# Performance work log

Hardware: AMD Instinct MI355X
Metric: run time of the kernel (lower is better)

Reference implementation:

```python
import jax, jax.numpy as jnp
import numpy as np

B, L, D_MODEL, HEADS, EXP, DEPTH = 2, 2048, 1024, 16, 2, 12
D_EXP = D_MODEL * EXP
D_HEAD = D_EXP // HEADS


def _layernorm(x, g, b, eps=1e-5):
    mu = jnp.mean(x, axis=-1, keepdims=True)
    var = jnp.mean(jnp.square(x - mu), axis=-1, keepdims=True)
    return (x - mu) * jax.lax.rsqrt(var + eps) * g + b


def setup_inputs() -> dict:
    key = jax.random.key(0)
    ks = jax.random.split(key, 4)
    x = jax.random.normal(ks[0], (B, L, D_MODEL), dtype=jnp.float32)
    w_in = jax.random.normal(ks[1], (D_MODEL, 4 * D_EXP), dtype=jnp.float32) * 0.02
    w_out = jax.random.normal(ks[2], (D_EXP, D_MODEL), dtype=jnp.float32) * (0.02 / np.sqrt(2 * DEPTH))
    return {
        "x": x,
        "ln1_g": jnp.ones((D_MODEL,), jnp.float32),
        "ln1_b": jnp.zeros((D_MODEL,), jnp.float32),
        "ln2_g": jnp.ones((D_MODEL,), jnp.float32),
        "ln2_b": jnp.zeros((D_MODEL,), jnp.float32),
        "w_in": w_in,
        "w_out": w_out,
        "smear_factor": jnp.linspace(-6.0, 6.0, HEADS, dtype=jnp.float32),
        "log_scale": jnp.zeros((HEADS,), jnp.float32),
    }


def reference(x, ln1_g, ln1_b, ln2_g, ln2_b, w_in, w_out, smear_factor, log_scale):
    b, l, d = x.shape
    h = smear_factor.shape[0]
    d_exp = w_in.shape[1] // 4
    dh = d_exp // h

    qkvp = _layernorm(x, ln1_g, ln1_b) @ w_in  # [b, l, 4*d_exp]
    q, k, v, p = jnp.split(qkvp, 4, axis=-1)
    # 'b i (h d) -> b h i d'
    to_heads = lambda t: t.reshape(b, l, h, dh).transpose(0, 2, 1, 3)
    q, k, v = to_heads(q), to_heads(k), to_heads(v)

    # smeared keys: k_i <- (1-s)*k_i + s*k_{i-1}  (zero at i=0)
    smear = jax.nn.sigmoid(smear_factor)[None, :, None, None]
    k_prev = jnp.pad(k, ((0, 0), (0, 0), (1, 0), (0, 0)))[:, :, :-1, :]
    k = (1.0 - smear) * k + smear * k_prev

    # ALiBi-style additive mask: slope[h]*j on causal part, -1e10 above diag
    half = h // 2
    slopes = jnp.concatenate([2.0 ** jnp.linspace(0.0, -8.0, half), jnp.zeros((h - half,), jnp.float32)])
    j = jnp.arange(l)
    causal = jnp.where(j[None, :] > j[:, None], jnp.float32(-1e10), jnp.float32(0.0))  # [l, l]
    mask = slopes[:, None, None] * j[None, None, :].astype(jnp.float32) + causal[None, :, :]  # [h, l, l]

    # SDPA with q/s, k/s and default scale 1/sqrt(dh): logits = q k^T / (s^2 sqrt(dh))
    inv = 1.0 / (jnp.exp(2.0 * log_scale)[None, :, None, None] * jnp.sqrt(jnp.float32(dh)))
    logits = jnp.einsum('bhid,bhjd->bhij', q, k) * inv + mask[None]
    attn = jax.nn.softmax(logits, axis=-1)
    o = jnp.einsum('bhij,bhjd->bhid', attn, v)
    o = o.transpose(0, 2, 1, 3).reshape(b, l, h * dh)  # 'b h i d -> b i (h d)'

    out = (jax.nn.silu(p) * o) @ w_out
    return _layernorm(out, ln2_g, ln2_b)
```

## Files before the change

### kernel.cpp

```cpp
#include <hip/hip_runtime.h>

typedef unsigned short u16;
typedef __attribute__((ext_vector_type(8))) short bf16x8;
typedef __attribute__((ext_vector_type(8))) unsigned short u16x8;
typedef __attribute__((ext_vector_type(4))) float f32x4;

#define L_SEQ 2048
#define NTOK 4096
#define DMODEL 1024
#define DEXP 2048
#define NH 16
#define DH 128

__device__ __forceinline__ u16 f2bf(float f) {
    unsigned u = __float_as_uint(f);
    unsigned r = (u + 0x7FFFu + ((u >> 16) & 1u)) >> 16;
    return (u16)r;
}
__device__ __forceinline__ float bf2f(u16 h) {
    return __uint_as_float(((unsigned)h) << 16);
}

template <int CTRL>
__device__ __forceinline__ float dpp_f(float x) {
    return __int_as_float(__builtin_amdgcn_update_dpp(0, __float_as_int(x), CTRL, 0xF, 0xF, true));
}
__device__ __forceinline__ float red16_max(float x) {
    x = fmaxf(x, dpp_f<0xB1>(x));
    x = fmaxf(x, dpp_f<0x4E>(x));
    x = fmaxf(x, dpp_f<0x124>(x));
    x = fmaxf(x, dpp_f<0x128>(x));
    return x;
}

__device__ __forceinline__ void gl_lds16(const u16* g, u16* l) {
    __builtin_amdgcn_global_load_lds((const __attribute__((address_space(1))) void*)g,
                                     (__attribute__((address_space(3))) void*)l, 16, 0, 0);
}

__global__ void conv_transpose(const float* __restrict__ in, u16* __restrict__ out, int R, int C) {
    __shared__ unsigned tile[32][33];
    int c0 = blockIdx.x * 32, r0 = blockIdx.y * 32;
    int tx = threadIdx.x, ty = threadIdx.y;
    for (int j = 0; j < 32; j += 8)
        tile[ty + j][tx] = (unsigned)f2bf(in[(size_t)(r0 + ty + j) * C + c0 + tx]);
    __syncthreads();
    for (int j = 0; j < 32; j += 8)
        out[(size_t)(c0 + ty + j) * R + r0 + tx] = (u16)tile[tx][ty + j];
}

__global__ __launch_bounds__(256) void ln_fwd(const float* __restrict__ x, const float* __restrict__ g,
                                              const float* __restrict__ bta, void* __restrict__ outp,
                                              int out_bf16) {
    int row = blockIdx.x;
    int t = threadIdx.x;
    const float* xr = x + (size_t)row * DMODEL;
    float4 xv = *(const float4*)&xr[t * 4];
    float s = xv.x + xv.y + xv.z + xv.w;
    float s2 = xv.x * xv.x + xv.y * xv.y + xv.z * xv.z + xv.w * xv.w;
    for (int off = 32; off >= 1; off >>= 1) {
        s += __shfl_xor(s, off);
        s2 += __shfl_xor(s2, off);
    }
    __shared__ float red[10];
    int w = t >> 6;
    if ((t & 63) == 0) { red[w] = s; red[4 + w] = s2; }
    __syncthreads();
    if (t == 0) {
        red[8] = red[0] + red[1] + red[2] + red[3];
        red[9] = red[4] + red[5] + red[6] + red[7];
    }
    __syncthreads();
    float mu = red[8] * (1.0f / DMODEL);
    float var = red[9] * (1.0f / DMODEL) - mu * mu;
    float rstd = rsqrtf(var + 1e-5f);
    float vals[4] = {xv.x, xv.y, xv.z, xv.w};
    for (int e = 0; e < 4; e++) {
        int c = t * 4 + e;
        float y = (vals[e] - mu) * rstd * g[c] + bta[c];
        if (out_bf16) ((u16*)outp)[(size_t)row * DMODEL + c] = f2bf(y);
        else          ((float*)outp)[(size_t)row * DMODEL + c] = y;
    }
}

__device__ __forceinline__ void store_out(u16* C, size_t idx, float v) { C[idx] = f2bf(v); }
__device__ __forceinline__ void store_out(float* C, size_t idx, float v) { C[idx] = v; }

template <typename OutT>
__global__ __launch_bounds__(256) void gemm_bt(const u16* __restrict__ A, const u16* __restrict__ BT,
                                               OutT* __restrict__ C, int M, int N, int K) {
    __shared__ u16 a_s[4096];
    __shared__ u16 b_s[4096];
    int tid = threadIdx.x;
    int m0 = blockIdx.y * 128, n0 = blockIdx.x * 128;
    int w = tid >> 6, lane = tid & 63, quad = lane >> 4, ln = lane & 15;
    int wr = (w >> 1) * 64, wc = (w & 1) * 64;
    f32x4 zero4 = {0.f, 0.f, 0.f, 0.f};
    f32x4 acc[4][4];
    for (int r = 0; r < 4; r++)
        for (int c = 0; c < 4; c++) acc[r][c] = zero4;

    int lrow = lane >> 2, lseg = (lane & 3) * 8;
    const u16* Ag0 = A + (size_t)(m0 + 32 * w + lrow) * K + lseg;
    const u16* Ag1 = Ag0 + (size_t)16 * K;
    const u16* Bg0 = BT + (size_t)(n0 + 32 * w + lrow) * K + lseg;
    const u16* Bg1 = Bg0 + (size_t)16 * K;
    u16* al0 = &a_s[(2 * w) * 512];
    u16* al1 = &a_s[(2 * w + 1) * 512];
    u16* bl0 = &b_s[(2 * w) * 512];
    u16* bl1 = &b_s[(2 * w + 1) * 512];

    for (int k0 = 0; k0 < K; k0 += 32) {
        __syncthreads();
        gl_lds16(Ag0 + k0, al0);
        gl_lds16(Ag1 + k0, al1);
        gl_lds16(Bg0 + k0, bl0);
        gl_lds16(Bg1 + k0, bl1);
        __syncthreads();
        bf16x8 af[4], bfr[4];
        for (int r = 0; r < 4; r++) af[r]  = *(const bf16x8*)&a_s[(wr + r * 16 + ln) * 32 + quad * 8];
        for (int c = 0; c < 4; c++) bfr[c] = *(const bf16x8*)&b_s[(wc + c * 16 + ln) * 32 + quad * 8];
        for (int r = 0; r < 4; r++)
            for (int c = 0; c < 4; c++)
                acc[r][c] = __builtin_amdgcn_mfma_f32_16x16x32_bf16(af[r], bfr[c], acc[r][c], 0, 0, 0);
    }
    for (int r = 0; r < 4; r++)
        for (int c = 0; c < 4; c++)
            for (int e = 0; e < 4; e++) {
                int row = m0 + wr + r * 16 + quad * 4 + e;
                int col = n0 + wc + c * 16 + ln;
                store_out(C, (size_t)row * N + col, acc[r][c][e]);
            }
}

__global__ __launch_bounds__(256) void smear_kernel(const u16* __restrict__ qkvp,
                                                    const float* __restrict__ smear_f,
                                                    u16* __restrict__ k_sm) {
    int gid = blockIdx.x * 256 + threadIdx.x;
    int base = gid * 8;
    int bl = base >> 11;
    int c = base & 2047;
    int h = c >> 7;
    int d = c & 127;
    int l = bl & (L_SEQ - 1);
    int bb = bl >> 11;
    float s = 1.0f / (1.0f + __expf(-smear_f[h]));
    u16x8 cur = *(const u16x8*)&qkvp[(size_t)bl * 8192 + 2048 + c];
    u16x8 prv = {0, 0, 0, 0, 0, 0, 0, 0};
    if (l > 0) prv = *(const u16x8*)&qkvp[(size_t)(bl - 1) * 8192 + 2048 + c];
    u16x8 outv;
    for (int u = 0; u < 8; u++) {
        float kc = bf2f(cur[u]);
        float kp = bf2f(prv[u]);
        outv[u] = f2bf((1.0f - s) * kc + s * kp);
    }
    *(u16x8*)&k_sm[(((size_t)(bb * 16 + h)) * L_SEQ + l) * DH + d] = outv;
}

__global__ void vT_kernel(const u16* __restrict__ qkvp, u16* __restrict__ v_t) {
    __shared__ unsigned tile[32][33];
    int l0 = blockIdx.x * 32, d0 = blockIdx.y * 32;
    int bh = blockIdx.z;
    int bb = bh >> 4, h = bh & 15;
    int tx = threadIdx.x, ty = threadIdx.y;
    size_t tokb = (size_t)bb * L_SEQ;
    for (int j = 0; j < 32; j += 8)
        tile[ty + j][tx] = (unsigned)qkvp[(tokb + l0 + ty + j) * 8192 + 4096 + h * DH + d0 + tx];
    __syncthreads();
    for (int j = 0; j < 32; j += 8)
        v_t[((size_t)bh * DH + d0 + ty + j) * L_SEQ + l0 + tx] = (u16)tile[tx][ty + j];
}

__global__ __launch_bounds__(256) void attn_kernel(const u16* __restrict__ qkvp,
                                                   const u16* __restrict__ k_sm,
                                                   const u16* __restrict__ v_t,
                                                   u16* __restrict__ ag2,
                                                   const float* __restrict__ log_scale) {
    __shared__ u16 k_s[8192];
    __shared__ u16 vt_s[8192];
    __shared__ u16 p_s[4608];
    int tid = threadIdx.x;
    int bh = blockIdx.y;
    int bb = bh >> 4, h = bh & 15;
    int w = tid >> 6, lane = tid & 63, quad = lane >> 4, ln = lane & 15;
    size_t tokb = (size_t)bb * L_SEQ;

    const float LOG2E = 1.44269504f;
    float inv = 1.0f / (__expf(2.0f * log_scale[h]) * sqrtf((float)DH));
    float scl = inv * LOG2E;
    float slope2 = ((h < 8) ? exp2f(-8.0f * (float)h / 7.0f) : 0.0f) * LOG2E;

    int lrow = lane >> 2, lseg8 = (lane & 3) * 8;
    f32x4 zero4 = {0.f, 0.f, 0.f, 0.f};
    u16* pw = &p_s[w * 1152];
    const short ONE_BF = (short)0x3F80;
    bf16x8 ones = {ONE_BF, ONE_BF, ONE_BF, ONE_BF, ONE_BF, ONE_BF, ONE_BF, ONE_BF};

    for (int sidx = 0; sidx < 2; sidx++) {
        int ib = sidx == 0 ? (31 - (int)blockIdx.x) : (int)blockIdx.x;
        int i0 = ib * 64;
        int si = i0 + w * 16;

        bf16x8 qf[4];
        for (int kt = 0; kt < 4; kt++)
            qf[kt] = *(const bf16x8*)&qkvp[(tokb + si + ln) * 8192 + h * DH + kt * 32 + quad * 8];

        float m_i[4];
        for (int r = 0; r < 4; r++) m_i[r] = -1e30f;
        f32x4 o_acc[8], l_acc;
        for (int dt = 0; dt < 8; dt++) o_acc[dt] = zero4;
        l_acc = zero4;

        const u16* kg[4];
        for (int g = 0; g < 4; g++)
            kg[g] = k_sm + ((size_t)bh * L_SEQ + g * 16 + lrow) * DH + w * 32 + lseg8;
        const u16* vg[4];
        u16* vl[4];
        for (int q = 0; q < 4; q++) {
            int c = w * 4 + q;
            int jt = c >> 3, dg = c & 7;
            vg[q] = v_t + ((size_t)bh * DH + dg * 16 + lrow) * L_SEQ + jt * 32 + lseg8;
            vl[q] = &vt_s[jt * 4096 + dg * 512];
        }

        for (int j0 = 0; j0 <= i0; j0 += 64) {
            __syncthreads();
            for (int g = 0; g < 4; g++) {
                gl_lds16(kg[g], &k_s[w * 2048 + g * 512]);
                kg[g] += 64 * DH;
            }
            for (int q = 0; q < 4; q++) {
                gl_lds16(vg[q], vl[q]);
                vg[q] += 64;
            }
            __syncthreads();
            if (j0 > si + 15) continue;

            f32x4 sc[4];
            for (int ct = 0; ct < 4; ct++) sc[ct] = zero4;
            for (int kt = 0; kt < 4; kt++)
                for (int ct = 0; ct < 4; ct++) {
                    bf16x8 bfr = *(const bf16x8*)&k_s[kt * 2048 + (ct * 16 + ln) * 32 + quad * 8];
                    sc[ct] = __builtin_amdgcn_mfma_f32_16x16x32_bf16(qf[kt], bfr, sc[ct], 0, 0, 0);
                }

            bool full = (j0 + 63 <= si);
            float s2[4][4];
            float aj0 = slope2 * (float)(j0 + ln);
            for (int ct = 0; ct < 4; ct++) {
                float ajv = aj0 + slope2 * (float)(16 * ct);
                int j = j0 + ct * 16 + ln;
                for (int r = 0; r < 4; r++) {
                    float v = fmaf(sc[ct][r], scl, ajv);
                    if (!full) {
                        int i = si + quad * 4 + r;
                        if (j > i) v = -3.0e38f;
                    }
                    s2[ct][r] = v;
                }
            }
            float alpha[4];
            bool any_resc = false;
            for (int r = 0; r < 4; r++) {
                float mr = fmaxf(fmaxf(s2[0][r], s2[1][r]), fmaxf(s2[2][r], s2[3][r]));
                mr = red16_max(mr);
                float mnew = fmaxf(m_i[r], mr);
                alpha[r] = exp2f(m_i[r] - mnew);
                any_resc |= (alpha[r] != 1.0f);
                m_i[r] = mnew;
                for (int ct = 0; ct < 4; ct++) {
                    float p = exp2f(s2[ct][r] - mnew);
                    u16 pb = (u16)(__float_as_uint(p) >> 16);
                    pw[(quad * 4 + r) * 72 + ct * 16 + ln] = pb;
                }
            }
            if (__any(any_resc)) {
                for (int dt = 0; dt < 8; dt++) {
                    f32x4 o = o_acc[dt];
                    for (int r = 0; r < 4; r++) o[r] *= alpha[r];
                    o_acc[dt] = o;
                }
                for (int r = 0; r < 4; r++) l_acc[r] *= alpha[r];
            }
            asm volatile("s_waitcnt lgkmcnt(0)" ::: "memory");
            for (int ks = 0; ks < 2; ks++) {
                bf16x8 pa = *(const bf16x8*)&pw[ln * 72 + ks * 32 + quad * 8];
                l_acc = __builtin_amdgcn_mfma_f32_16x16x32_bf16(pa, ones, l_acc, 0, 0, 0);
                for (int dt = 0; dt < 8; dt++) {
                    bf16x8 vf = *(const bf16x8*)&vt_s[ks * 4096 + (dt * 16 + ln) * 32 + quad * 8];
                    o_acc[dt] = __builtin_amdgcn_mfma_f32_16x16x32_bf16(pa, vf, o_acc[dt], 0, 0, 0);
                }
            }
        }

        float rinv[4];
        for (int r = 0; r < 4; r++) rinv[r] = __builtin_amdgcn_rcpf(l_acc[r]);
        for (int dt = 0; dt < 8; dt++)
            for (int r = 0; r < 4; r++) {
                int i = si + quad * 4 + r;
                int dcol = dt * 16 + ln;
                float o = o_acc[dt][r] * rinv[r];
                float pv = bf2f(qkvp[(tokb + i) * 8192 + 6144 + h * DH + dcol]);
                float gate = pv * __builtin_amdgcn_rcpf(1.0f + exp2f(-pv * LOG2E));
                ag2[(tokb + i) * 2048 + h * DH + dcol] = f2bf(gate * o);
            }
    }
}

extern "C" void kernel_launch(void* const* d_in, const int* in_sizes, int n_in,
                              void* d_out, int out_size, void* d_ws, size_t ws_size,
                              hipStream_t stream) {
    const float* x       = (const float*)d_in[0];
    const float* ln1_g   = (const float*)d_in[1];
    const float* ln1_b   = (const float*)d_in[2];
    const float* ln2_g   = (const float*)d_in[3];
    const float* ln2_b   = (const float*)d_in[4];
    const float* w_in    = (const float*)d_in[5];
    const float* w_out   = (const float*)d_in[6];
    const float* smear_f = (const float*)d_in[7];
    const float* logsc   = (const float*)d_in[8];
    float* out = (float*)d_out;
    char* ws = (char*)d_ws;

    u16* w_inT   = (u16*)(ws + 0);
    u16* w_outT  = (u16*)(ws + (size_t)16777216);
    u16* lnA     = (u16*)(ws + (size_t)20971520);
    u16* qkvp    = (u16*)(ws + (size_t)29360128);
    u16* k_sm    = (u16*)(ws + (size_t)96468992);
    u16* ag2     = (u16*)(ws + (size_t)113246208);
    float* out_pre = (float*)(ws + (size_t)96468992);
    u16* v_t     = (u16*)(ws + 0);

    dim3 b32x8(32, 8);
    conv_transpose<<<dim3(8192 / 32, 1024 / 32), b32x8, 0, stream>>>(w_in, w_inT, 1024, 8192);
    conv_transpose<<<dim3(1024 / 32, 2048 / 32), b32x8, 0, stream>>>(w_out, w_outT, 2048, 1024);
    ln_fwd<<<NTOK, 256, 0, stream>>>(x, ln1_g, ln1_b, (void*)lnA, 1);
    gemm_bt<u16><<<dim3(8192 / 128, 4096 / 128), 256, 0, stream>>>(lnA, w_inT, qkvp, NTOK, 8192, 1024);
    smear_kernel<<<4096, 256, 0, stream>>>(qkvp, smear_f, k_sm);
    vT_kernel<<<dim3(L_SEQ / 32, DH / 32, 32), b32x8, 0, stream>>>(qkvp, v_t);
    attn_kernel<<<dim3(16, 32), 256, 0, stream>>>(qkvp, k_sm, v_t, ag2, logsc);
    gemm_bt<float><<<dim3(1024 / 128, 4096 / 128), 256, 0, stream>>>(ag2, w_outT, out_pre, NTOK, 1024, 2048);
    ln_fwd<<<NTOK, 256, 0, stream>>>(out_pre, ln2_g, ln2_b, (void*)out, 0);
}
```

Baseline: 387.4 us.

## Double-buffer K/V tiles in LDS with XOR swizzle and MFMA priority hints

The attention kernel now keeps two LDS buffers for the K and V^T tiles. It prefetches the next 64-key tile while computing on the current one, which removes one of the two barriers per iteration. It also XOR-swizzles the 8-element column segments in LDS, by changing the global source addresses and the read offsets, to cut bank conflicts on the fragment reads. s_setprio is raised around the MFMA loops. The cost is double the K/V LDS footprint, which may lower occupancy, and the early skip of fully masked wave tiles is gone.

```diff
diff --git a/kernel.cpp b/kernel.cpp
--- a/kernel.cpp
+++ b/kernel.cpp
@@ -176,8 +176,8 @@
                                                    const u16* __restrict__ v_t,
                                                    u16* __restrict__ ag2,
                                                    const float* __restrict__ log_scale) {
-    __shared__ u16 k_s[8192];
-    __shared__ u16 vt_s[8192];
+    __shared__ u16 k_s[16384];
+    __shared__ u16 vt_s[16384];
     __shared__ u16 p_s[4608];
     int tid = threadIdx.x;
     int bh = blockIdx.y;
@@ -190,7 +190,9 @@
     float scl = inv * LOG2E;
     float slope2 = ((h < 8) ? exp2f(-8.0f * (float)h / 7.0f) : 0.0f) * LOG2E;
 
-    int lrow = lane >> 2, lseg8 = (lane & 3) * 8;
+    int lrow = lane >> 2, lcol = lane & 3;
+    int lsw8 = (lcol ^ ((lrow >> 1) & 3)) * 8;
+    int qsw = (quad ^ ((ln >> 1) & 3)) * 8;
     f32x4 zero4 = {0.f, 0.f, 0.f, 0.f};
     u16* pw = &p_s[w * 1152];
     const short ONE_BF = (short)0x3F80;
@@ -213,36 +215,39 @@
 
         const u16* kg[4];
         for (int g = 0; g < 4; g++)
-            kg[g] = k_sm + ((size_t)bh * L_SEQ + g * 16 + lrow) * DH + w * 32 + lseg8;
+            kg[g] = k_sm + ((size_t)bh * L_SEQ + g * 16 + lrow) * DH + w * 32 + lsw8;
         const u16* vg[4];
-        u16* vl[4];
+        int vloff[4];
         for (int q = 0; q < 4; q++) {
             int c = w * 4 + q;
             int jt = c >> 3, dg = c & 7;
-            vg[q] = v_t + ((size_t)bh * DH + dg * 16 + lrow) * L_SEQ + jt * 32 + lseg8;
-            vl[q] = &vt_s[jt * 4096 + dg * 512];
+            vg[q] = v_t + ((size_t)bh * DH + dg * 16 + lrow) * L_SEQ + jt * 32 + lsw8;
+            vloff[q] = jt * 4096 + dg * 512;
         }
 
+        for (int g = 0; g < 4; g++) { gl_lds16(kg[g], &k_s[w * 2048 + g * 512]); kg[g] += 64 * DH; }
+        for (int q = 0; q < 4; q++) { gl_lds16(vg[q], &vt_s[vloff[q]]); vg[q] += 64; }
+        __syncthreads();
+
+        int cur = 0;
         for (int j0 = 0; j0 <= i0; j0 += 64) {
-            __syncthreads();
-            for (int g = 0; g < 4; g++) {
-                gl_lds16(kg[g], &k_s[w * 2048 + g * 512]);
-                kg[g] += 64 * DH;
-            }
-            for (int q = 0; q < 4; q++) {
-                gl_lds16(vg[q], vl[q]);
-                vg[q] += 64;
-            }
-            __syncthreads();
-            if (j0 > si + 15) continue;
+            if (j0 + 64 <= i0) {
+                int nb = (cur ^ 1) * 8192;
+                for (int g = 0; g < 4; g++) { gl_lds16(kg[g], &k_s[nb + w * 2048 + g * 512]); kg[g] += 64 * DH; }
+                for (int q = 0; q < 4; q++) { gl_lds16(vg[q], &vt_s[nb + vloff[q]]); vg[q] += 64; }
+            }
+            const u16* kb = &k_s[cur * 8192];
+            const u16* vb = &vt_s[cur * 8192];
 
             f32x4 sc[4];
             for (int ct = 0; ct < 4; ct++) sc[ct] = zero4;
+            __builtin_amdgcn_s_setprio(1);
             for (int kt = 0; kt < 4; kt++)
                 for (int ct = 0; ct < 4; ct++) {
-                    bf16x8 bfr = *(const bf16x8*)&k_s[kt * 2048 + (ct * 16 + ln) * 32 + quad * 8];
+                    bf16x8 bfr = *(const bf16x8*)&kb[kt * 2048 + (ct * 16 + ln) * 32 + qsw];
                     sc[ct] = __builtin_amdgcn_mfma_f32_16x16x32_bf16(qf[kt], bfr, sc[ct], 0, 0, 0);
                 }
+            __builtin_amdgcn_s_setprio(0);
 
             bool full = (j0 + 63 <= si);
             float s2[4][4];
@@ -283,14 +288,18 @@
                 for (int r = 0; r < 4; r++) l_acc[r] *= alpha[r];
             }
             asm volatile("s_waitcnt lgkmcnt(0)" ::: "memory");
+            __builtin_amdgcn_s_setprio(1);
             for (int ks = 0; ks < 2; ks++) {
                 bf16x8 pa = *(const bf16x8*)&pw[ln * 72 + ks * 32 + quad * 8];
                 l_acc = __builtin_amdgcn_mfma_f32_16x16x32_bf16(pa, ones, l_acc, 0, 0, 0);
                 for (int dt = 0; dt < 8; dt++) {
-                    bf16x8 vf = *(const bf16x8*)&vt_s[ks * 4096 + (dt * 16 + ln) * 32 + quad * 8];
+                    bf16x8 vf = *(const bf16x8*)&vb[ks * 4096 + (dt * 16 + ln) * 32 + qsw];
                     o_acc[dt] = __builtin_amdgcn_mfma_f32_16x16x32_bf16(pa, vf, o_acc[dt], 0, 0, 0);
                 }
             }
+            __builtin_amdgcn_s_setprio(0);
+            __syncthreads();
+            cur ^= 1;
         }
 
         float rinv[4];
```

New measurement: 395.1 us. About the same (+2.0%).
